# Kernel optimization log

Hardware: AMD Instinct MI355X
Metric: run time of the kernel (lower is better)

## Reference

```python
import jax, jax.numpy as jnp
import numpy as np
from jax import lax

# Orthonormal 2x2 Haar (db1). Analysis uses dwt_scale per coefficient; the
# synthesis uses 0.5*idwt_scale so that dwt_scale=0.5, idwt_scale=1.0 gives a
# perfect round trip (Hadamard matrix M, M@M = 4I, M symmetric).
DWT_SCALE = 0.5
IDWT_SCALE = 1.0
WT_LEVELS = 3
STRIDE = 1
PAD = 1  # (kernel_size - 1) // 2


def dwt2(x, s):
    # x: (B, C, H, W) -> (B, C, 4, H/2, W/2), subband order LL, LH, HL, HH
    a = x[..., 0::2, 0::2]
    b = x[..., 0::2, 1::2]
    c = x[..., 1::2, 0::2]
    d = x[..., 1::2, 1::2]
    ll = (a + b + c + d) * s
    lh = (a - b + c - d) * s
    hl = (a + b - c - d) * s
    hh = (a - b - c + d) * s
    return jnp.stack([ll, lh, hl, hh], axis=2)


def idwt2(sub, s):
    # sub: (B, C, 4, h, w) -> (B, C, 2h, 2w); inverse of dwt2 when s = 0.5/ (4*dwt_s) * ... here Hadamard symmetric
    ll, lh, hl, hh = sub[:, :, 0], sub[:, :, 1], sub[:, :, 2], sub[:, :, 3]
    a = (ll + lh + hl + hh) * s
    b = (ll - lh + hl - hh) * s
    c = (ll + lh - hl - hh) * s
    d = (ll - lh - hl + hh) * s
    B, C, h, w = a.shape
    row0 = jnp.stack([a, b], axis=-1).reshape(B, C, h, 2 * w)
    row1 = jnp.stack([c, d], axis=-1).reshape(B, C, h, 2 * w)
    return jnp.stack([row0, row1], axis=-2).reshape(B, C, 2 * h, 2 * w)


def conv2d(x, w, stride, pad):
    return lax.conv_general_dilated(
        x, w, window_strides=(stride, stride),
        padding=[(pad, pad), (pad, pad)],
        dimension_numbers=('NCHW', 'OIHW', 'NCHW'))


def wtconv_core(x, weight):
    cout4 = weight.shape[0]
    cout = cout4 // 4
    curr_ll = x
    ll_levels, high_levels = [], []
    for _ in range(WT_LEVELS):
        sub = dwt2(curr_ll, DWT_SCALE)             # (B, C, 4, h, w)
        B, C, _, h, w = sub.shape
        y = conv2d(sub.reshape(B, C * 4, h, w), weight, STRIDE, PAD)
        y = y.reshape(B, cout, 4, h, w)
        ll_levels.append(y[:, :, 0])
        high_levels.append(y[:, :, 1:])
        curr_ll = sub[:, :, 0]                     # pre-conv LL feeds next level
    next_ll = jnp.zeros_like(ll_levels[-1])
    for ll, hi in zip(reversed(ll_levels), reversed(high_levels)):
        ll = ll + next_ll
        sub = jnp.concatenate([ll[:, :, None], hi], axis=2)
        next_ll = idwt2(sub, 0.5 * IDWT_SCALE)
    return next_ll


def setup_inputs() -> dict:
    key = jax.random.key(0)
    k1, k2, k3 = jax.random.split(key, 3)
    B, C, H, W = 8, 32, 224, 224
    K = 3
    x = jax.random.normal(k1, (B, C, H, W), dtype=jnp.float32)
    fan_in = C * 4 * K * K
    bound = np.sqrt(6.0 / ((1.0 + 2.236 ** 2) * fan_in))
    weight = jax.random.uniform(k2, (C * 4, C * 4, K, K), dtype=jnp.float32,
                                minval=-bound, maxval=bound)
    bias = jax.random.normal(k3, (C,), dtype=jnp.float32) * 0.01
    return {"x": x, "weight": weight, "bias": bias}


def reference(x, weight, bias):
    H, W = x.shape[-2:]
    pad_factor = 2 ** WT_LEVELS
    pad_h = (pad_factor - H % pad_factor) % pad_factor
    pad_w = (pad_factor - W % pad_factor) % pad_factor
    xp = x
    if pad_h > 0 or pad_w > 0:
        xp = jnp.pad(x, ((0, 0), (0, 0), (0, pad_h), (0, pad_w)), mode='reflect')
    out = wtconv_core(xp, weight)
    out = out[..., :H, :W]
    return out + bias[None, :, None, None]
```

## Files before the change

### kernel.cpp

```cpp
#include <hip/hip_runtime.h>

typedef __bf16 bf16_t;
typedef __bf16 bf16x4_t __attribute__((ext_vector_type(4)));
typedef __bf16 bf16x8_t __attribute__((ext_vector_type(8)));
typedef float f32x16_t __attribute__((ext_vector_type(16)));

#define AS_G(p) ((const __attribute__((address_space(1))) void*)(p))
#define AS_L(p) ((__attribute__((address_space(3))) void*)(p))
#define DRAIN_VM() asm volatile("s_waitcnt vmcnt(0)" ::: "memory")

__device__ __forceinline__ void repack_body(const float* __restrict__ w,
                                            bf16_t* __restrict__ wt2,
                                            int o) {
  int e = o & 7;
  int lane = (o >> 3) & 63;
  int f = o >> 9;
  int wc = f & 1;
  int nt = (f >> 1) & 1;
  int kc = (f >> 2) & 3;
  int hk = (f >> 4) & 1;
  int t = f >> 5;
  int oc = wc * 64 + nt * 32 + (lane & 31);
  int ic = (hk * 8 + kc * 2 + (lane >> 5)) * 8 + e;
  wt2[o] = (bf16_t)w[((size_t)oc * 128 + ic) * 9 + t];
}

__device__ __forceinline__ void dwt_body(const float* __restrict__ in,
                                         bf16_t* __restrict__ sub,
                                         float* __restrict__ llout,
                                         int h, int w, bf16_t* lds) {
  const int bi = blockIdx.z;
  const int i = blockIdx.y;
  const int j0 = blockIdx.x * 64;
  const int tid = threadIdx.x;
  const int j = tid & 63;
  const int cg = tid >> 6;
  const int jg = j0 + j;
  const bool jok = jg < w;
  const int H2 = h * 2, W2 = w * 2;
  for (int c = cg; c < 32; c += 4) {
    float va = 0.f, vb = 0.f, vc = 0.f, vd = 0.f;
    if (jok) {
      const float2* p0 = (const float2*)(in + ((size_t)(bi * 32 + c) * H2 + 2 * i) * W2);
      const float2* p1 = (const float2*)(in + ((size_t)(bi * 32 + c) * H2 + 2 * i + 1) * W2);
      float2 r0 = p0[jg];
      float2 r1 = p1[jg];
      va = r0.x; vb = r0.y; vc = r1.x; vd = r1.y;
    }
    float ll = (va + vb + vc + vd) * 0.5f;
    float lh = (va - vb + vc - vd) * 0.5f;
    float hl = (va + vb - vc - vd) * 0.5f;
    float hh = (va - vb - vc + vd) * 0.5f;
    bf16x4_t q;
    q.x = (bf16_t)ll; q.y = (bf16_t)lh; q.z = (bf16_t)hl; q.w = (bf16_t)hh;
    *(bf16x4_t*)(&lds[j * 132 + c * 4]) = q;
    if (llout != nullptr && jok)
      llout[((size_t)(bi * 32 + c) * h + i) * w + jg] = ll;
  }
  __syncthreads();
  const size_t obase = ((size_t)bi * h + i) * w;
  for (int it = 0; it < 8; ++it) {
    int flat = it * 256 + tid;
    int jj = flat >> 5;
    int c4 = flat & 31;
    if (j0 + jj < w) {
      bf16x4_t q = *(const bf16x4_t*)(&lds[jj * 132 + c4 * 4]);
      *(bf16x4_t*)(sub + ((obase + j0 + jj) << 7) + c4 * 4) = q;
    }
  }
}

__global__ __launch_bounds__(256) void dwt0_kernel(const float* __restrict__ in,
                                                   bf16_t* __restrict__ sub,
                                                   float* __restrict__ llout,
                                                   const float* __restrict__ wsrc,
                                                   bf16_t* __restrict__ wt2,
                                                   int h, int w) {
  __shared__ __align__(16) bf16_t lds[64 * 132];
  if (blockIdx.z == 8) {
    int bid = blockIdx.y * 2 + blockIdx.x;
    for (int o = bid * 256 + threadIdx.x; o < 147456; o += 224 * 256)
      repack_body(wsrc, wt2, o);
    return;
  }
  dwt_body(in, sub, llout, h, w, lds);
}

__global__ __launch_bounds__(256) void dwt_kernel(const float* __restrict__ in,
                                                  bf16_t* __restrict__ sub,
                                                  float* __restrict__ llout,
                                                  int h, int w) {
  __shared__ __align__(16) bf16_t lds[64 * 132];
  dwt_body(in, sub, llout, h, w, lds);
}

__device__ __forceinline__ void conv_idwt_tile(
    const bf16_t* __restrict__ sub, const bf16_t* __restrict__ wt2,
    const float* __restrict__ nll, const float* __restrict__ nllup,
    const float* __restrict__ bias, float* __restrict__ out,
    int h, int w, int bi, int y0, int x0, int och, uint4* smemV) {
  char* haloS = (char*)smemV;
  char* Bbuf = (char*)smemV + 23040;
  float* scr = (float*)((char*)smemV + 23040);
  const int tid = threadIdx.x;
  const size_t img_base = (size_t)bi * h * w;

  const int lane = tid & 63;
  const int wv = tid >> 6;
  const int m = lane & 31;
  const int hw_ = lane >> 5;
  const int il = wv * 2 + (m >> 4);
  const int jl = m & 15;
  const int pixA = il * 18 + jl;

  f32x16_t acc[2] = {};

  for (int hk = 0; hk < 2; ++hk) {
    if (hk) __syncthreads();
    for (int it = 0; it < 6; ++it) {
      int flat = it * 256 + tid;
      int pix = flat >> 3;
      int ch = flat & 7;
      if (pix < 180) {
        int r = pix / 18;
        int c = pix - r * 18;
        int gy = y0 + r - 1;
        int gx = x0 + c - 1;
        uint4 v = make_uint4(0u, 0u, 0u, 0u);
        if ((unsigned)gy < (unsigned)h && (unsigned)gx < (unsigned)w)
          v = *(const uint4*)(sub + ((img_base + (size_t)gy * w + gx) << 7) +
                              ((hk * 8 + ch) << 3));
        *(uint4*)(haloS + (pix << 7) + ((ch ^ (pix & 7)) << 4)) = v;
      }
    }
    {
      const int th0 = hk;
#pragma unroll
      for (int q = 0; q < 2; ++q) {
        const bf16_t* srcp = wt2 + (((th0 << 4) + (wv << 2) + (q << 1) + och) << 9) + (lane << 3);
        __builtin_amdgcn_global_load_lds(AS_G(srcp),
            AS_L(Bbuf + (((wv << 1) + q) << 10)), 16, 0, 0);
      }
    }
    DRAIN_VM();
    __syncthreads();

    int cur = 0;
    for (int t = 0; t < 9; ++t) {
      if (t < 8) {
        const int thn = ((t + 1) << 1) + hk;
#pragma unroll
        for (int q = 0; q < 2; ++q) {
          const bf16_t* srcp = wt2 + (((thn << 4) + (wv << 2) + (q << 1) + och) << 9) + (lane << 3);
          __builtin_amdgcn_global_load_lds(AS_G(srcp),
              AS_L(Bbuf + ((cur ^ 1) << 13) + (((wv << 1) + q) << 10)), 16, 0, 0);
        }
      }
      const int ky = t / 3;
      const int kx = t - ky * 3;
      const int pix0 = pixA + ky * 18 + kx;
      const int s0 = pix0 & 7;
      const char* hp0 = haloS + (pix0 << 7);
      const char* bp = Bbuf + (cur << 13) + (lane << 4);
#pragma unroll
      for (int kc = 0; kc < 4; ++kc) {
        bf16x8_t b0 = *(const bf16x8_t*)(bp + ((kc << 1) << 10));
        bf16x8_t b1 = *(const bf16x8_t*)(bp + (((kc << 1) + 1) << 10));
        const int cidx = kc * 2 + hw_;
        bf16x8_t a0 = *(const bf16x8_t*)(hp0 + ((cidx ^ s0) << 4));
        acc[0] = __builtin_amdgcn_mfma_f32_32x32x16_bf16(a0, b0, acc[0], 0, 0, 0);
        acc[1] = __builtin_amdgcn_mfma_f32_32x32x16_bf16(a0, b1, acc[1], 0, 0, 0);
      }
      DRAIN_VM();
      __syncthreads();
      cur ^= 1;
    }
  }

  const int W2 = w * 2;
  const int H2 = h * 2;
  const int hu = h >> 1, wu = w >> 1;
  const int mh_t = m >> 4;
  const int mm = m & 15;
  const int kw = mm >> 2;
  const int sw = mm & 3;

#pragma unroll
  for (int ph = 0; ph < 4; ++ph) {
    const int nt = ph >> 1;
    const int mh = ph & 1;
    if (ph) __syncthreads();
    if (mh_t == mh) {
#pragma unroll
      for (int reg = 0; reg < 16; ++reg) {
        int row = (reg & 3) + ((reg >> 2) << 3) + (hw_ << 2);
        int px = wv * 32 + row;
        scr[px * 17 + (kw << 2) + sw] = acc[nt][reg];
      }
    }
    __syncthreads();
#pragma unroll
    for (int it = 0; it < 2; ++it) {
      int idx = it * 256 + tid;
      int ox4 = idx & 7;
      int dy = (idx >> 3) & 1;
      int row = (idx >> 4) & 7;
      int k = (idx >> 7) & 3;
      int gy = y0 + row;
      int gx = x0 + ox4 * 2;
      if (gy >= h || gx >= w) continue;
      int p0 = row * 16 + ox4 * 2;
      int p1 = p0 + 1;
      float4 sa = *(const float4*)(&scr[p0 * 17 + (k << 2)]);
      float4 sb = *(const float4*)(&scr[p1 * 17 + (k << 2)]);
      float sg = dy ? -1.f : 1.f;
      float e0 = sa.x + sa.y + sg * (sa.z + sa.w);
      float e1 = sa.x - sa.y + sg * (sa.z - sa.w);
      float e2 = sb.x + sb.y + sg * (sb.z + sb.w);
      float e3 = sb.x - sb.y + sg * (sb.z - sb.w);
      int ch = och * 16 + nt * 8 + mh * 4 + k;
      float n0 = 0.f, n1 = 0.f;
      if (nll != nullptr) {
        const float* np = nll + ((size_t)(bi * 32 + ch) * h + gy) * w + gx;
        float2 nv = *(const float2*)np;
        n0 = nv.x; n1 = nv.y;
      }
      if (nllup != nullptr) {
        float u = nllup[((size_t)(bi * 32 + ch) * hu + (gy >> 1)) * wu + (gx >> 1)];
        n0 += 0.5f * u;
        n1 += 0.5f * u;
      }
      float bv = (bias != nullptr) ? bias[ch] : 0.f;
      float4 o;
      o.x = 0.5f * e0 + 0.5f * n0 + bv;
      o.y = 0.5f * e1 + 0.5f * n0 + bv;
      o.z = 0.5f * e2 + 0.5f * n1 + bv;
      o.w = 0.5f * e3 + 0.5f * n1 + bv;
      float* op = out + ((size_t)(bi * 32 + ch) * H2 + 2 * gy + dy) * W2 + 2 * gx;
      *(float4*)op = o;
    }
  }
}

__global__ __launch_bounds__(256, 4) void conv_idwt_kernel(
    const bf16_t* __restrict__ sub, const bf16_t* __restrict__ wt2,
    const float* __restrict__ nll, const float* __restrict__ nllup,
    const float* __restrict__ bias, float* __restrict__ out, int h, int w) {
  __shared__ uint4 smemV[2464];
  conv_idwt_tile(sub, wt2, nll, nllup, bias, out, h, w,
                 blockIdx.z, blockIdx.y * 8, (blockIdx.x >> 1) * 16,
                 blockIdx.x & 1, smemV);
}

__global__ __launch_bounds__(256, 4) void conv12_kernel(
    const bf16_t* __restrict__ sub1, const bf16_t* __restrict__ sub2,
    const bf16_t* __restrict__ wt2, float* __restrict__ nll1raw,
    float* __restrict__ nll2) {
  __shared__ uint4 smemV[2464];
  const int B = blockIdx.x;
  const bf16_t* sub;
  float* outp;
  int hh, bi, by, bx, och;
  if (B < 448) {
    och = B & 1;
    int q = B >> 1;
    bx = q & 3;
    int r = q >> 2;
    by = r % 7;
    bi = r / 7;
    sub = sub1; outp = nll1raw; hh = 56;
  } else {
    int lb = B - 448;
    och = lb & 1;
    int q = lb >> 1;
    bx = q & 1;
    int r = q >> 1;
    by = r & 3;
    bi = r >> 2;
    sub = sub2; outp = nll2; hh = 28;
  }
  conv_idwt_tile(sub, wt2, nullptr, nullptr, nullptr, outp, hh, hh,
                 bi, by * 8, bx * 16, och, smemV);
}

extern "C" void kernel_launch(void* const* d_in, const int* in_sizes, int n_in,
                              void* d_out, int out_size, void* d_ws, size_t ws_size,
                              hipStream_t stream) {
  if (ws_size < 66125824u) return;

  const float* x = (const float*)d_in[0];
  const float* weight = (const float*)d_in[1];
  const float* bias = (const float*)d_in[2];
  float* out = (float*)d_out;
  char* ws = (char*)d_ws;

  bf16_t* wt2 = (bf16_t*)(ws);
  bf16_t* sub0 = (bf16_t*)(ws + 294912);
  bf16_t* sub1 = (bf16_t*)(ws + 25985024);
  bf16_t* sub2 = (bf16_t*)(ws + 32407552);
  float* ll0 = (float*)(ws + 34013184);
  float* ll1 = (float*)(ws + 46858240);
  float* nll2 = (float*)(ws + 50069504);
  float* nll1 = (float*)(ws + 53280768);

  dwt0_kernel<<<dim3(2, 112, 9), 256, 0, stream>>>(x, sub0, ll0, weight, wt2, 112, 112);
  dwt_kernel<<<dim3(1, 56, 8), 256, 0, stream>>>(ll0, sub1, ll1, 56, 56);
  dwt_kernel<<<dim3(1, 28, 8), 256, 0, stream>>>(ll1, sub2, nullptr, 28, 28);
  conv12_kernel<<<576, 256, 0, stream>>>(sub1, sub2, wt2, nll1, nll2);
  conv_idwt_kernel<<<dim3(14, 14, 8), 256, 0, stream>>>(sub0, wt2, nll1, nll2, bias, out, 112, 112);
}
```

Before: 188.0 us.

## Triple-buffer weight tiles with prefetch distance two and partial vmcnt waits

Moves the per-tap weight staging from a double buffer with full vmcnt(0) drains to a triple buffer that prefetches two taps ahead. Each step waits only with vmcnt(2), so the most recent prefetch can stay in flight while the MFMAs run. Plain __syncthreads is replaced by s_barrier plus sched_barrier, and the loop is fully unrolled. Shared memory per block grows by about 8 KB to hold the third buffer, which may lower occupancy at 4 blocks per CU.

```diff
diff --git a/kernel.cpp b/kernel.cpp
--- a/kernel.cpp
+++ b/kernel.cpp
@@ -7,7 +7,6 @@
 
 #define AS_G(p) ((const __attribute__((address_space(1))) void*)(p))
 #define AS_L(p) ((__attribute__((address_space(3))) void*)(p))
-#define DRAIN_VM() asm volatile("s_waitcnt vmcnt(0)" ::: "memory")
 
 __device__ __forceinline__ void repack_body(const float* __restrict__ w,
                                             bf16_t* __restrict__ wt2,
@@ -133,27 +132,30 @@
         *(uint4*)(haloS + (pix << 7) + ((ch ^ (pix & 7)) << 4)) = v;
       }
     }
-    {
-      const int th0 = hk;
+#pragma unroll
+    for (int pf = 0; pf < 2; ++pf) {
+      const int th = pf * 2 + hk;
 #pragma unroll
       for (int q = 0; q < 2; ++q) {
-        const bf16_t* srcp = wt2 + (((th0 << 4) + (wv << 2) + (q << 1) + och) << 9) + (lane << 3);
+        const bf16_t* srcp = wt2 + (((th << 4) + (wv << 2) + (q << 1) + och) << 9) + (lane << 3);
         __builtin_amdgcn_global_load_lds(AS_G(srcp),
-            AS_L(Bbuf + (((wv << 1) + q) << 10)), 16, 0, 0);
-      }
-    }
-    DRAIN_VM();
-    __syncthreads();
-
-    int cur = 0;
+            AS_L(Bbuf + (pf << 13) + (((wv << 1) + q) << 10)), 16, 0, 0);
+      }
+    }
+    asm volatile("s_waitcnt vmcnt(2) lgkmcnt(0)" ::: "memory");
+    __builtin_amdgcn_sched_barrier(0);
+    __builtin_amdgcn_s_barrier();
+
+#pragma unroll
     for (int t = 0; t < 9; ++t) {
-      if (t < 8) {
-        const int thn = ((t + 1) << 1) + hk;
+      if (t < 7) {
+        const int thn = ((t + 2) << 1) + hk;
+        const int bn = (t + 2) % 3;
 #pragma unroll
         for (int q = 0; q < 2; ++q) {
           const bf16_t* srcp = wt2 + (((thn << 4) + (wv << 2) + (q << 1) + och) << 9) + (lane << 3);
           __builtin_amdgcn_global_load_lds(AS_G(srcp),
-              AS_L(Bbuf + ((cur ^ 1) << 13) + (((wv << 1) + q) << 10)), 16, 0, 0);
+              AS_L(Bbuf + (bn << 13) + (((wv << 1) + q) << 10)), 16, 0, 0);
         }
       }
       const int ky = t / 3;
@@ -161,7 +163,7 @@
       const int pix0 = pixA + ky * 18 + kx;
       const int s0 = pix0 & 7;
       const char* hp0 = haloS + (pix0 << 7);
-      const char* bp = Bbuf + (cur << 13) + (lane << 4);
+      const char* bp = Bbuf + ((t % 3) << 13) + (lane << 4);
 #pragma unroll
       for (int kc = 0; kc < 4; ++kc) {
         bf16x8_t b0 = *(const bf16x8_t*)(bp + ((kc << 1) << 10));
@@ -171,9 +173,13 @@
         acc[0] = __builtin_amdgcn_mfma_f32_32x32x16_bf16(a0, b0, acc[0], 0, 0, 0);
         acc[1] = __builtin_amdgcn_mfma_f32_32x32x16_bf16(a0, b1, acc[1], 0, 0, 0);
       }
-      DRAIN_VM();
-      __syncthreads();
-      cur ^= 1;
+      if (t < 7) {
+        asm volatile("s_waitcnt vmcnt(2)" ::: "memory");
+      } else if (t == 7) {
+        asm volatile("s_waitcnt vmcnt(0)" ::: "memory");
+      }
+      __builtin_amdgcn_sched_barrier(0);
+      __builtin_amdgcn_s_barrier();
     }
   }
 
@@ -246,7 +252,7 @@
     const bf16_t* __restrict__ sub, const bf16_t* __restrict__ wt2,
     const float* __restrict__ nll, const float* __restrict__ nllup,
     const float* __restrict__ bias, float* __restrict__ out, int h, int w) {
-  __shared__ uint4 smemV[2464];
+  __shared__ uint4 smemV[2976];
   conv_idwt_tile(sub, wt2, nll, nllup, bias, out, h, w,
                  blockIdx.z, blockIdx.y * 8, (blockIdx.x >> 1) * 16,
                  blockIdx.x & 1, smemV);
@@ -256,7 +262,7 @@
     const bf16_t* __restrict__ sub1, const bf16_t* __restrict__ sub2,
     const bf16_t* __restrict__ wt2, float* __restrict__ nll1raw,
     float* __restrict__ nll2) {
-  __shared__ uint4 smemV[2464];
+  __shared__ uint4 smemV[2976];
   const int B = blockIdx.x;
   const bf16_t* sub;
   float* outp;
```

New measurement: 195.2 us. 1.04x slower.

## Split level-0 DWT: compute LL early, fold full subband write into conv12 launch

Applied to the files above, without the earlier changes.

The first kernel now computes only the fp32 LL output of level 0, plus the weight repack, so the dependent level-1/2 DWTs can start sooner. The full bf16 level-0 subband write is moved into extra blocks appended to the conv12 launch, overlapping it with the small level-1/2 convolutions that underfill the GPU. The cost is that x is read twice from global memory, and conv12s blocks now mix two workload types.

```diff
diff --git a/kernel.cpp b/kernel.cpp
--- a/kernel.cpp
+++ b/kernel.cpp
@@ -28,10 +28,8 @@
 __device__ __forceinline__ void dwt_body(const float* __restrict__ in,
                                          bf16_t* __restrict__ sub,
                                          float* __restrict__ llout,
-                                         int h, int w, bf16_t* lds) {
-  const int bi = blockIdx.z;
-  const int i = blockIdx.y;
-  const int j0 = blockIdx.x * 64;
+                                         int h, int w, int bi, int i, int j0,
+                                         bf16_t* lds) {
   const int tid = threadIdx.x;
   const int j = tid & 63;
   const int cg = tid >> 6;
@@ -70,20 +68,31 @@
   }
 }
 
-__global__ __launch_bounds__(256) void dwt0_kernel(const float* __restrict__ in,
-                                                   bf16_t* __restrict__ sub,
+__global__ __launch_bounds__(256) void ll0r_kernel(const float* __restrict__ in,
                                                    float* __restrict__ llout,
                                                    const float* __restrict__ wsrc,
                                                    bf16_t* __restrict__ wt2,
                                                    int h, int w) {
-  __shared__ __align__(16) bf16_t lds[64 * 132];
   if (blockIdx.z == 8) {
     int bid = blockIdx.y * 2 + blockIdx.x;
     for (int o = bid * 256 + threadIdx.x; o < 147456; o += 224 * 256)
       repack_body(wsrc, wt2, o);
     return;
   }
-  dwt_body(in, sub, llout, h, w, lds);
+  const int bi = blockIdx.z;
+  const int i = blockIdx.y;
+  const int jg = blockIdx.x * 64 + (threadIdx.x & 63);
+  const int cg = threadIdx.x >> 6;
+  if (jg >= w) return;
+  const int H2 = h * 2, W2 = w * 2;
+  for (int c = cg; c < 32; c += 4) {
+    const float2* p0 = (const float2*)(in + ((size_t)(bi * 32 + c) * H2 + 2 * i) * W2);
+    const float2* p1 = (const float2*)(in + ((size_t)(bi * 32 + c) * H2 + 2 * i + 1) * W2);
+    float2 r0 = p0[jg];
+    float2 r1 = p1[jg];
+    llout[((size_t)(bi * 32 + c) * h + i) * w + jg] =
+        (r0.x + r0.y + r1.x + r1.y) * 0.5f;
+  }
 }
 
 __global__ __launch_bounds__(256) void dwt_kernel(const float* __restrict__ in,
@@ -91,7 +100,7 @@
                                                   float* __restrict__ llout,
                                                   int h, int w) {
   __shared__ __align__(16) bf16_t lds[64 * 132];
-  dwt_body(in, sub, llout, h, w, lds);
+  dwt_body(in, sub, llout, h, w, blockIdx.z, blockIdx.y, blockIdx.x * 64, lds);
 }
 
 __device__ __forceinline__ void conv_idwt_tile(
@@ -252,12 +261,22 @@
                  blockIdx.x & 1, smemV);
 }
 
-__global__ __launch_bounds__(256, 4) void conv12_kernel(
+__global__ __launch_bounds__(256, 4) void conv12s_kernel(
+    const float* __restrict__ x, bf16_t* __restrict__ sub0,
     const bf16_t* __restrict__ sub1, const bf16_t* __restrict__ sub2,
     const bf16_t* __restrict__ wt2, float* __restrict__ nll1raw,
     float* __restrict__ nll2) {
   __shared__ uint4 smemV[2464];
   const int B = blockIdx.x;
+  if (B >= 576) {
+    int r = B - 576;
+    int bx = r & 1;
+    int rr = r >> 1;
+    int i = rr % 112;
+    int bi = rr / 112;
+    dwt_body(x, sub0, nullptr, 112, 112, bi, i, bx * 64, (bf16_t*)smemV);
+    return;
+  }
   const bf16_t* sub;
   float* outp;
   int hh, bi, by, bx, och;
@@ -303,9 +322,9 @@
   float* nll2 = (float*)(ws + 50069504);
   float* nll1 = (float*)(ws + 53280768);
 
-  dwt0_kernel<<<dim3(2, 112, 9), 256, 0, stream>>>(x, sub0, ll0, weight, wt2, 112, 112);
+  ll0r_kernel<<<dim3(2, 112, 9), 256, 0, stream>>>(x, ll0, weight, wt2, 112, 112);
   dwt_kernel<<<dim3(1, 56, 8), 256, 0, stream>>>(ll0, sub1, ll1, 56, 56);
   dwt_kernel<<<dim3(1, 28, 8), 256, 0, stream>>>(ll1, sub2, nullptr, 28, 28);
-  conv12_kernel<<<576, 256, 0, stream>>>(sub1, sub2, wt2, nll1, nll2);
+  conv12s_kernel<<<2368, 256, 0, stream>>>(x, sub0, sub1, sub2, wt2, nll1, nll2);
   conv_idwt_kernel<<<dim3(14, 14, 8), 256, 0, stream>>>(sub0, wt2, nll1, nll2, bias, out, 112, 112);
 }
```

After: 181.4 us. -3.5%, faster.
